# Performance work log

Hardware: AMD Instinct MI355X
Metric: run time of the kernel (lower is better)

The kernel has to match this reference:

```python
import jax, jax.numpy as jnp
import numpy as np

EPS = 1e-8
C_RGLRU = 8.0  # Griffin constant

def rmsnorm(x, w):
    rms = jnp.sqrt(jnp.mean(x * x, axis=-1, keepdims=True) + EPS)
    return w * (x / rms)

def causal_depthwise_conv(x, conv_w, conv_b):
    # x: [B,S,H], conv_w: [K,H] depthwise causal conv, left-padded
    K = conv_w.shape[0]
    S = x.shape[1]
    xp = jnp.pad(x, ((0, 0), (K - 1, 0), (0, 0)))
    y = sum(conv_w[k] * xp[:, k:k + S, :] for k in range(K))
    return y + conv_b

def rg_lru(x, ga_W, ga_b, gx_W, gx_b, a_param):
    # x: [B,S,H]. Griffin RG-LRU: h_t = a_t h_{t-1} + sqrt(1-a_t^2) (i_t * x_t)
    r = jax.nn.sigmoid(x @ ga_W + ga_b)          # recurrence gate
    i = jax.nn.sigmoid(x @ gx_W + gx_b)          # input gate
    log_a = -C_RGLRU * jax.nn.softplus(a_param) * r
    a = jnp.exp(log_a)
    mult = jnp.sqrt(-jnp.expm1(2.0 * log_a))     # sqrt(1 - a^2), stable
    b = mult * (i * x)
    def combine(c1, c2):
        a1, b1 = c1
        a2, b2 = c2
        return a1 * a2, a2 * b1 + b2
    _, h = jax.lax.associative_scan(combine, (a, b), axis=1)
    return h

def setup_inputs() -> dict:
    D, H, F, K, B, S = 2048, 2048, 6144, 4, 2, 2048
    key = jax.random.key(0)
    ks = jax.random.split(key, 16)
    def lin(k, fan_in, shape):
        return jax.random.normal(k, shape, jnp.float32) * (fan_in ** -0.5)
    return {
        "x": jax.random.normal(ks[0], (B, S, D), jnp.float32),
        "norm1_w": jnp.ones((D,), jnp.float32),
        "left_W": lin(ks[1], D, (D, H)), "left_b": jnp.zeros((H,), jnp.float32),
        "right_W": lin(ks[2], D, (D, H)), "right_b": jnp.zeros((H,), jnp.float32),
        "conv_w": lin(ks[3], K, (K, H)), "conv_b": jnp.zeros((H,), jnp.float32),
        "ga_W": lin(ks[4], H, (H, H)), "ga_b": jnp.zeros((H,), jnp.float32),
        "gx_W": lin(ks[5], H, (H, H)), "gx_b": jnp.zeros((H,), jnp.float32),
        "a_param": jax.random.uniform(ks[6], (H,), jnp.float32, 0.5, 3.0),
        "out_W": lin(ks[7], H, (H, D)), "out_b": jnp.zeros((D,), jnp.float32),
        "norm2_w": jnp.ones((D,), jnp.float32),
        "up1_W": lin(ks[8], D, (D, F)), "up1_b": jnp.zeros((F,), jnp.float32),
        "up2_W": lin(ks[9], D, (D, F)), "up2_b": jnp.zeros((F,), jnp.float32),
        "down_W": lin(ks[10], F, (F, D)), "down_b": jnp.zeros((D,), jnp.float32),
    }

def reference(x, norm1_w, left_W, left_b, right_W, right_b, conv_w, conv_b,
              ga_W, ga_b, gx_W, gx_b, a_param, out_W, out_b,
              norm2_w, up1_W, up1_b, up2_W, up2_b, down_W, down_b):
    gelu = lambda t: jax.nn.gelu(t, approximate=False)
    # recurrent sub-block (pre-norm residual)
    xn = rmsnorm(x, norm1_w)
    left = gelu(xn @ left_W + left_b)
    right = rg_lru(causal_depthwise_conv(xn @ right_W + right_b, conv_w, conv_b),
                   ga_W, ga_b, gx_W, gx_b, a_param)
    x1 = (left * right) @ out_W + out_b + x
    # gated MLP sub-block (pre-norm residual)
    x1n = rmsnorm(x1, norm2_w)
    mlp = (gelu(x1n @ up1_W + up1_b) * (x1n @ up2_W + up2_b)) @ down_W + down_b
    return mlp + x1
```

## Files before the change

### kernel.cpp

```cpp
#include <hip/hip_runtime.h>
#include <cstdint>
#include <cstdio>

typedef __bf16 bf16x8 __attribute__((ext_vector_type(8)));
typedef float  f32x4  __attribute__((ext_vector_type(4)));
typedef const __attribute__((address_space(1))) void* gas_ptr;
typedef __attribute__((address_space(3))) void* las_ptr;

__device__ __forceinline__ uint16_t f32_to_bf16_rne(float f){
  uint32_t u = __builtin_bit_cast(uint32_t, f);
  u += 0x7FFFu + ((u >> 16) & 1u);
  return (uint16_t)(u >> 16);
}
__device__ __forceinline__ float bf16_to_f32(uint16_t h){
  uint32_t u = (uint32_t)h << 16;
  return __builtin_bit_cast(float, u);
}
__device__ __forceinline__ float gelu_exact(float x){
  return 0.5f * x * (1.f + erff(x * 0.7071067811865475f));
}

template<int EPI>
__device__ __forceinline__ void epi_store(float v, size_t idx, int row, int col,
    int N, int SPLIT, const float* auxF, const uint16_t* auxB,
    float* Cf, uint16_t* Cb0, uint16_t* Cb1, bool second)
{
  if constexpr (EPI == 1) {
    if (!second) Cb0[(size_t)row * SPLIT + col] = f32_to_bf16_rne(gelu_exact(v));
    else         Cb1[(size_t)row * (N - SPLIT) + (col - SPLIT)] = f32_to_bf16_rne(v);
  }
  if constexpr (EPI == 2) Cb0[idx] = f32_to_bf16_rne(v);
  if constexpr (EPI == 4) Cb0[idx] = f32_to_bf16_rne(v + auxF[idx]);
  if constexpr (EPI == 5) Cf[idx] = v + bf16_to_f32(auxB[idx]);
}

template<int EPI, int BM>
__global__ __launch_bounds__(512)
void gemm8p(const uint16_t* __restrict__ A, const uint16_t* __restrict__ Bt,
            const float* __restrict__ bias0, const float* __restrict__ bias1,
            const float* __restrict__ auxF, const uint16_t* __restrict__ auxB,
            float* __restrict__ Cf, uint16_t* __restrict__ Cb0, uint16_t* __restrict__ Cb1,
            int M, int N, int K, int SPLIT)
{
  constexpr int BN = 256;
  constexpr int M_REP   = BM / 32;
  constexpr int MH      = M_REP / 2;
  constexpr int LOADS_A = BM / 64;
  constexpr int LOADS_B = BN / 64;
  constexpr int LTOT    = LOADS_A + LOADS_B;
  constexpr int ASIZE   = BM * 128;
  constexpr int ABYTES  = 2 * ASIZE;
  constexpr int BSIZE   = BN * 128;
  __shared__ alignas(16) char smem[2 * (BM + BN) * 128];

  const int tid = threadIdx.x, lane = tid & 63, wid = tid >> 6;
  const int wm = wid >> 2, wn = wid & 3;
  const int la = lane & 15, lq = lane >> 4;
  const int n0 = blockIdx.x * BN, m0 = blockIdx.y * BM;

  const int rt = tid >> 3;
  const int gs = (tid & 7) ^ (rt & 7);
  const uint16_t* srcA = A  + (size_t)(m0 + rt) * K + gs * 8;
  const uint16_t* srcB = Bt + (size_t)(n0 + rt) * K + gs * 8;

  const int rowAb = (wm * (BM / 2) + la) * 128;
  const int rowBb = (wn * 64 + la) * 128;
  const int ck0 = ((lq)     ^ (la & 7)) * 16;
  const int ck1 = ((4 + lq) ^ (la & 7)) * 16;

  f32x4 acc[M_REP][4];
  const f32x4 fz = {0.f, 0.f, 0.f, 0.f};
#pragma unroll
  for (int m = 0; m < M_REP; ++m)
#pragma unroll
    for (int n = 0; n < 4; ++n) acc[m][n] = fz;

  bf16x8 aF[MH][2], bF0[2][2], bF1[2][2];
  const int NT = K >> 6;

#define STAGE_A8(KT, BUF) do { _Pragma("unroll")                              \
    for (int l = 0; l < LOADS_A; ++l)                                         \
      __builtin_amdgcn_global_load_lds(                                       \
          (gas_ptr)(srcA + (size_t)(KT) * 64 + (size_t)l * 64 * K),           \
          (las_ptr)(smem + (BUF) * ASIZE + (l * 512 + tid) * 16), 16, 0, 0);  \
  } while (0)
#define STAGE_B8(KT, BUF) do { _Pragma("unroll")                              \
    for (int l = 0; l < LOADS_B; ++l)                                         \
      __builtin_amdgcn_global_load_lds(                                       \
          (gas_ptr)(srcB + (size_t)(KT) * 64 + (size_t)l * 64 * K),           \
          (las_ptr)(smem + ABYTES + (BUF) * BSIZE + (l * 512 + tid) * 16),    \
          16, 0, 0);                                                          \
  } while (0)
#define RD_B8(DST, NH, BUF) do { _Pragma("unroll")                            \
    for (int nq = 0; nq < 2; ++nq) {                                          \
      int ro_ = ABYTES + (BUF) * BSIZE + rowBb + ((NH) * 2 + nq) * 2048;      \
      DST[nq][0] = *(const bf16x8*)(smem + ro_ + ck0);                        \
      DST[nq][1] = *(const bf16x8*)(smem + ro_ + ck1);                        \
    }                                                                         \
  } while (0)
#define RD_A8(MHS, BUF) do { _Pragma("unroll")                                \
    for (int mq = 0; mq < MH; ++mq) {                                         \
      int ro_ = (BUF) * ASIZE + rowAb + ((MHS) * MH + mq) * 2048;             \
      aF[mq][0] = *(const bf16x8*)(smem + ro_ + ck0);                         \
      aF[mq][1] = *(const bf16x8*)(smem + ro_ + ck1);                         \
    }                                                                         \
  } while (0)
#define MM8(MHS, NH, BF) do { _Pragma("unroll")                               \
    for (int mq = 0; mq < MH; ++mq)                                           \
      _Pragma("unroll")                                                       \
      for (int nq = 0; nq < 2; ++nq) {                                        \
        acc[(MHS)*MH+mq][(NH)*2+nq] = __builtin_amdgcn_mfma_f32_16x16x32_bf16(\
            aF[mq][0], BF[nq][0], acc[(MHS)*MH+mq][(NH)*2+nq], 0, 0, 0);      \
        acc[(MHS)*MH+mq][(NH)*2+nq] = __builtin_amdgcn_mfma_f32_16x16x32_bf16(\
            aF[mq][1], BF[nq][1], acc[(MHS)*MH+mq][(NH)*2+nq], 0, 0, 0);      \
      }                                                                       \
  } while (0)
#define BARR() __builtin_amdgcn_s_barrier()

  STAGE_A8(0, 0); STAGE_B8(0, 0);
  STAGE_A8(1, 1); STAGE_B8(1, 1);
  asm volatile("s_waitcnt vmcnt(%0)" :: "i"(LTOT) : "memory");
  BARR();

  for (int t = 0; t < NT; ++t) {
    const int buf = t & 1;
    const bool pf = (t + 2 < NT);
    RD_B8(bF0, 0, buf); RD_A8(0, buf);
    asm volatile("s_waitcnt lgkmcnt(8)" ::: "memory");
    BARR();
    __builtin_amdgcn_s_setprio(1); MM8(0, 0, bF0); __builtin_amdgcn_s_setprio(0);
    BARR();
    RD_B8(bF1, 1, buf);
    BARR();
    __builtin_amdgcn_s_setprio(1); MM8(0, 1, bF1); __builtin_amdgcn_s_setprio(0);
    BARR();
    RD_A8(1, buf);
    if (pf) STAGE_B8(t + 2, buf);
    BARR();
    __builtin_amdgcn_s_setprio(1); MM8(1, 0, bF0); __builtin_amdgcn_s_setprio(0);
    BARR();
    if (pf) STAGE_A8(t + 2, buf);
    BARR();
    __builtin_amdgcn_s_setprio(1); MM8(1, 1, bF1); __builtin_amdgcn_s_setprio(0);
    if (pf) asm volatile("s_waitcnt vmcnt(%0)" :: "i"(LTOT) : "memory");
    else    asm volatile("s_waitcnt vmcnt(0)" ::: "memory");
    BARR();
  }
#undef STAGE_A8
#undef STAGE_B8
#undef RD_B8
#undef RD_A8
#undef MM8
#undef BARR

  if constexpr (EPI == 6) {
    const int GN = N >> 1;
#pragma unroll
    for (int np = 0; np < 2; ++np) {
      int gcol = (n0 >> 1) + wn * 32 + np * 16 + la;
      float b1 = bias0[gcol], b2 = bias1[gcol];
#pragma unroll
      for (int m = 0; m < M_REP; ++m) {
        int rbase = m0 + wm * (BM / 2) + m * 16 + lq * 4;
#pragma unroll
        for (int r = 0; r < 4; ++r) {
          int row = rbase + r;
          float v1 = acc[m][2*np][r] + b1;
          float v2 = acc[m][2*np+1][r] + b2;
          Cb0[(size_t)row * GN + gcol] = f32_to_bf16_rne(gelu_exact(v1) * v2);
        }
      }
    }
  } else {
#pragma unroll
    for (int n = 0; n < 4; ++n) {
      int col = n0 + wn * 64 + n * 16 + la;
      const bool second = (col >= SPLIT);
      float bv = second ? bias1[col - SPLIT] : bias0[col];
#pragma unroll
      for (int m = 0; m < M_REP; ++m) {
        int rbase = m0 + wm * (BM / 2) + m * 16 + lq * 4;
#pragma unroll
        for (int r = 0; r < 4; ++r) {
          int row = rbase + r;
          size_t idx = (size_t)row * N + col;
          epi_store<EPI>(acc[m][n][r] + bv, idx, row, col, N, SPLIT, auxF, auxB, Cf, Cb0, Cb1, second);
        }
      }
    }
  }
}

template<int EPI, int BM>
__global__ __launch_bounds__(512)
void gemm2p(const uint16_t* __restrict__ A, const uint16_t* __restrict__ Bt,
            const float* __restrict__ bias0, const float* __restrict__ bias1,
            const float* __restrict__ auxF, const uint16_t* __restrict__ auxB,
            float* __restrict__ Cf, uint16_t* __restrict__ Cb0, uint16_t* __restrict__ Cb1,
            int M, int N, int K, int SPLIT)
{
  constexpr int BN = 256;
  constexpr int M_REP   = BM / 32;
  constexpr int LOADS_A = BM / 64;
  constexpr int LOADS_B = BN / 64;
  constexpr int ABYTES  = 2 * BM * 128;
  __shared__ alignas(16) char smem[2 * (BM + BN) * 128];

  const int tid  = threadIdx.x;
  const int lane = tid & 63;
  const int wid  = tid >> 6;
  const int wm = wid >> 2, wn = wid & 3;
  const int la = lane & 15, lq = lane >> 4;
  const int n0 = blockIdx.x * BN;
  const int m0 = blockIdx.y * BM;

  const int rt = tid >> 3;
  const int gs = (tid & 7) ^ (rt & 7);
  const uint16_t* srcA = A  + (size_t)(m0 + rt) * K + gs * 8;
  const uint16_t* srcB = Bt + (size_t)(n0 + rt) * K + gs * 8;

  const int rowAb = (wm * (BM / 2) + la) * 128;
  const int rowBb = (wn * 64 + la) * 128;
  const int ck0 = ((lq)     ^ (la & 7)) * 16;
  const int ck1 = ((4 + lq) ^ (la & 7)) * 16;

  f32x4 acc[M_REP][4];
  const f32x4 fz = {0.f, 0.f, 0.f, 0.f};
#pragma unroll
  for (int m = 0; m < M_REP; ++m)
#pragma unroll
    for (int n = 0; n < 4; ++n) acc[m][n] = fz;

  const int NT = K >> 6;

#define STAGE(KT, BUF) do {                                                   \
    const uint16_t* sa_ = srcA + (size_t)(KT) * 64;                           \
    const uint16_t* sb_ = srcB + (size_t)(KT) * 64;                           \
    _Pragma("unroll")                                                         \
    for (int l = 0; l < LOADS_A; ++l)                                         \
      __builtin_amdgcn_global_load_lds((gas_ptr)(sa_ + (size_t)l * 64 * K),   \
          (las_ptr)(smem + (BUF) * BM * 128 + (l * 512 + tid) * 16), 16, 0, 0);\
    _Pragma("unroll")                                                         \
    for (int l = 0; l < LOADS_B; ++l)                                         \
      __builtin_amdgcn_global_load_lds((gas_ptr)(sb_ + (size_t)l * 64 * K),   \
          (las_ptr)(smem + ABYTES + (BUF) * BN * 128 + (l * 512 + tid) * 16), \
          16, 0, 0);                                                          \
  } while (0)

  STAGE(0, 0);
  asm volatile("s_waitcnt vmcnt(0)" ::: "memory");
  __builtin_amdgcn_s_barrier();

  int cur = 0;
  for (int kt = 0; kt < NT; ++kt) {
    const bool pf = (kt + 1 < NT);
    if (pf) STAGE(kt + 1, cur ^ 1);

    const int offA = cur * BM * 128;
    const int offB = ABYTES + cur * BN * 128;

    bf16x8 bF[4][2];
#pragma unroll
    for (int n = 0; n < 4; ++n) {
      int ro = offB + rowBb + n * 2048;
      bF[n][0] = *(const bf16x8*)(smem + ro + ck0);
      bF[n][1] = *(const bf16x8*)(smem + ro + ck1);
    }
    __builtin_amdgcn_s_setprio(1);
#pragma unroll
    for (int m = 0; m < M_REP; ++m) {
      int ro = offA + rowAb + m * 2048;
      bf16x8 a0 = *(const bf16x8*)(smem + ro + ck0);
      bf16x8 a1 = *(const bf16x8*)(smem + ro + ck1);
#pragma unroll
      for (int n = 0; n < 4; ++n) {
        acc[m][n] = __builtin_amdgcn_mfma_f32_16x16x32_bf16(a0, bF[n][0], acc[m][n], 0, 0, 0);
        acc[m][n] = __builtin_amdgcn_mfma_f32_16x16x32_bf16(a1, bF[n][1], acc[m][n], 0, 0, 0);
      }
    }
    __builtin_amdgcn_s_setprio(0);

    if (pf) {
      asm volatile("s_waitcnt vmcnt(0)" ::: "memory");
      __builtin_amdgcn_s_barrier();
      cur ^= 1;
    }
  }
#undef STAGE

#pragma unroll
  for (int n = 0; n < 4; ++n) {
    int col = n0 + wn * 64 + n * 16 + la;
    const bool second = (col >= SPLIT);
    float bv = second ? bias1[col - SPLIT] : bias0[col];
#pragma unroll
    for (int m = 0; m < M_REP; ++m) {
      int rbase = m0 + wm * (BM / 2) + m * 16 + lq * 4;
#pragma unroll
      for (int r = 0; r < 4; ++r) {
        int row = rbase + r;
        size_t idx = (size_t)row * N + col;
        epi_store<EPI>(acc[m][n][r] + bv, idx, row, col, N, SPLIT, auxF, auxB, Cf, Cb0, Cb1, second);
      }
    }
  }
}

__global__ __launch_bounds__(256)
void cvt_transpose(const float* __restrict__ in, uint16_t* __restrict__ out, int R, int C)
{
  __shared__ float tile[64][65];
  const int r0 = blockIdx.y * 64, c0 = blockIdx.x * 64;
  const int t = threadIdx.x;
  const int lc = (t & 15) * 4;
  const int lr0 = t >> 4;
#pragma unroll
  for (int j = 0; j < 4; j++){
    int lr = lr0 + j*16;
    float4 v = *(const float4*)(in + (size_t)(r0 + lr) * C + c0 + lc);
    tile[lr][lc+0] = v.x; tile[lr][lc+1] = v.y; tile[lr][lc+2] = v.z; tile[lr][lc+3] = v.w;
  }
  __syncthreads();
  const int oc = t >> 2;
  const int rseg = (t & 3) * 16;
  alignas(16) uint16_t tmp[16];
#pragma unroll
  for (int j = 0; j < 16; j++) tmp[j] = f32_to_bf16_rne(tile[rseg + j][oc]);
  uint4* dst = (uint4*)(out + (size_t)(c0 + oc) * R + r0 + rseg);
  dst[0] = *(const uint4*)(&tmp[0]);
  dst[1] = *(const uint4*)(&tmp[8]);
}

__global__ __launch_bounds__(256)
void cvt_transpose_ileave(const float* __restrict__ in, uint16_t* __restrict__ out,
                          int R, int C, int half)
{
  __shared__ float tile[64][65];
  const int r0 = blockIdx.y * 64, c0 = blockIdx.x * 64;
  const int t = threadIdx.x;
  const int lc = (t & 15) * 4;
  const int lr0 = t >> 4;
#pragma unroll
  for (int j = 0; j < 4; j++){
    int lr = lr0 + j*16;
    float4 v = *(const float4*)(in + (size_t)(r0 + lr) * C + c0 + lc);
    tile[lr][lc+0] = v.x; tile[lr][lc+1] = v.y; tile[lr][lc+2] = v.z; tile[lr][lc+3] = v.w;
  }
  __syncthreads();
  const int oc = t >> 2;
  const int rseg = (t & 3) * 16;
  const int c = c0 + oc;
  const int wrow = ((c >> 4) << 5) + half * 16 + (c & 15);
  alignas(16) uint16_t tmp[16];
#pragma unroll
  for (int j = 0; j < 16; j++) tmp[j] = f32_to_bf16_rne(tile[rseg + j][oc]);
  uint4* dst = (uint4*)(out + (size_t)wrow * R + r0 + rseg);
  dst[0] = *(const uint4*)(&tmp[0]);
  dst[1] = *(const uint4*)(&tmp[8]);
}

__global__ __launch_bounds__(256)
void rmsnorm_kernel(const float* __restrict__ x, const float* __restrict__ w,
                    uint16_t* __restrict__ out, int D)
{
  const int row = blockIdx.x;
  const float* xr = x + (size_t)row * D;
  const int base = threadIdx.x * 8;
  float4 va = *(const float4*)(xr + base);
  float4 vb = *(const float4*)(xr + base + 4);
  float ss = va.x*va.x + va.y*va.y + va.z*va.z + va.w*va.w
           + vb.x*vb.x + vb.y*vb.y + vb.z*vb.z + vb.w*vb.w;
#pragma unroll
  for (int o = 32; o > 0; o >>= 1) ss += __shfl_xor(ss, o);
  __shared__ float red[4];
  if ((threadIdx.x & 63) == 0) red[threadIdx.x >> 6] = ss;
  __syncthreads();
  float tot = red[0] + red[1] + red[2] + red[3];
  float inv = rsqrtf(tot / (float)D + 1e-8f);
  float4 wa = *(const float4*)(w + base);
  float4 wb = *(const float4*)(w + base + 4);
  alignas(16) uint16_t tmp[8];
  tmp[0] = f32_to_bf16_rne(va.x * wa.x * inv);
  tmp[1] = f32_to_bf16_rne(va.y * wa.y * inv);
  tmp[2] = f32_to_bf16_rne(va.z * wa.z * inv);
  tmp[3] = f32_to_bf16_rne(va.w * wa.w * inv);
  tmp[4] = f32_to_bf16_rne(vb.x * wb.x * inv);
  tmp[5] = f32_to_bf16_rne(vb.y * wb.y * inv);
  tmp[6] = f32_to_bf16_rne(vb.z * wb.z * inv);
  tmp[7] = f32_to_bf16_rne(vb.w * wb.w * inv);
  *(uint4*)(out + (size_t)row * D + base) = *(const uint4*)tmp;
}

__global__ __launch_bounds__(256)
void rmsnorm_bf16_kernel(const uint16_t* __restrict__ x, const float* __restrict__ w,
                         uint16_t* __restrict__ out, int D)
{
  const int row = blockIdx.x;
  const uint16_t* xr = x + (size_t)row * D;
  const int base = threadIdx.x * 8;
  uint4 v = *(const uint4*)(xr + base);
  const uint16_t* vp = (const uint16_t*)&v;
  float xs[8];
  float ss = 0.f;
#pragma unroll
  for (int j = 0; j < 8; ++j){ xs[j] = bf16_to_f32(vp[j]); ss += xs[j]*xs[j]; }
#pragma unroll
  for (int o = 32; o > 0; o >>= 1) ss += __shfl_xor(ss, o);
  __shared__ float red[4];
  if ((threadIdx.x & 63) == 0) red[threadIdx.x >> 6] = ss;
  __syncthreads();
  float tot = red[0] + red[1] + red[2] + red[3];
  float inv = rsqrtf(tot / (float)D + 1e-8f);
  float4 wa = *(const float4*)(w + base);
  float4 wb = *(const float4*)(w + base + 4);
  float wv[8] = {wa.x, wa.y, wa.z, wa.w, wb.x, wb.y, wb.z, wb.w};
  alignas(16) uint16_t tmp[8];
#pragma unroll
  for (int j = 0; j < 8; ++j) tmp[j] = f32_to_bf16_rne(xs[j] * wv[j] * inv);
  *(uint4*)(out + (size_t)row * D + base) = *(const uint4*)tmp;
}

__global__ __launch_bounds__(256)
void conv_kernel(const uint16_t* __restrict__ xin, const float* __restrict__ cw,
                 const float* __restrict__ cb, uint16_t* __restrict__ yout,
                 int S, int H)
{
  const int h = blockIdx.x * 256 + threadIdx.x;
  const int b = blockIdx.z;
  const int t0 = blockIdx.y * 128;
  const float w0 = cw[h], w1 = cw[H + h], w2 = cw[2*H + h], w3 = cw[3*H + h];
  const float bias = cb[h];
  const size_t colbase = (size_t)b * S * H + h;
  float xm3 = (t0 >= 3) ? bf16_to_f32(xin[colbase + (size_t)(t0-3)*H]) : 0.f;
  float xm2 = (t0 >= 2) ? bf16_to_f32(xin[colbase + (size_t)(t0-2)*H]) : 0.f;
  float xm1 = (t0 >= 1) ? bf16_to_f32(xin[colbase + (size_t)(t0-1)*H]) : 0.f;
  for (int t = t0; t < t0 + 128; ++t){
    size_t idx = colbase + (size_t)t * H;
    float xt = bf16_to_f32(xin[idx]);
    float y = w0*xm3 + w1*xm2 + w2*xm1 + w3*xt + bias;
    yout[idx] = f32_to_bf16_rne(y);
    xm3 = xm2; xm2 = xm1; xm1 = xt;
  }
}

__device__ __forceinline__ void rglru_ab(float rp, float ip, float xc, float coef,
                                         float& a, float& bb)
{
  float r  = 1.f / (1.f + expf(-rp));
  float la = coef * r;
  a = expf(la);
  float mult = sqrtf(-expm1f(2.f * la));
  float ig = 1.f / (1.f + expf(-ip));
  bb = mult * ig * xc;
}

__global__ __launch_bounds__(256)
void scan_phase1(const uint16_t* __restrict__ gpre, const uint16_t* __restrict__ convb,
                 const float* __restrict__ ap,
                 float* __restrict__ SA, float* __restrict__ SB,
                 int S, int H, int T0, int NC)
{
  const int h = blockIdx.x * 256 + threadIdx.x;
  const int j = blockIdx.y, b = blockIdx.z;
  const float coef = -8.f * log1pf(expf(ap[h]));
  size_t rowb = (size_t)b * S + (size_t)j * T0;
  float A = 1.f, Bc = 0.f;
  for (int t = 0; t < T0; ++t){
    size_t row = rowb + t;
    float rp = bf16_to_f32(gpre[row * 2 * H + h]);
    float ip = bf16_to_f32(gpre[row * 2 * H + H + h]);
    float xc = bf16_to_f32(convb[row * H + h]);
    float a, bb; rglru_ab(rp, ip, xc, coef, a, bb);
    A *= a; Bc = a * Bc + bb;
  }
  size_t o = ((size_t)b * NC + j) * H + h;
  SA[o] = A; SB[o] = Bc;
}

__global__ __launch_bounds__(256)
void scan_phase2(const float* __restrict__ SA, const float* __restrict__ SB,
                 float* __restrict__ SH, int H, int NC)
{
  const int h = blockIdx.x * 256 + threadIdx.x;
  const int b = blockIdx.y;
  float hh = 0.f;
  for (int j = 0; j < NC; ++j){
    size_t o = ((size_t)b * NC + j) * H + h;
    SH[o] = hh;
    hh = SA[o] * hh + SB[o];
  }
}

__global__ __launch_bounds__(256)
void scan_phase3(const uint16_t* __restrict__ gpre, const uint16_t* __restrict__ convb,
                 const float* __restrict__ ap, const float* __restrict__ SH,
                 const uint16_t* __restrict__ left, uint16_t* __restrict__ lr,
                 int S, int H, int T0, int NC)
{
  const int h = blockIdx.x * 256 + threadIdx.x;
  const int j = blockIdx.y, b = blockIdx.z;
  const float coef = -8.f * log1pf(expf(ap[h]));
  float hh = SH[((size_t)b * NC + j) * H + h];
  size_t rowb = (size_t)b * S + (size_t)j * T0;
  for (int t = 0; t < T0; ++t){
    size_t row = rowb + t;
    float rp = bf16_to_f32(gpre[row * 2 * H + h]);
    float ip = bf16_to_f32(gpre[row * 2 * H + H + h]);
    float xc = bf16_to_f32(convb[row * H + h]);
    float a, bb; rglru_ab(rp, ip, xc, coef, a, bb);
    hh = a * hh + bb;
    lr[row * H + h] = f32_to_bf16_rne(bf16_to_f32(left[row * H + h]) * hh);
  }
}

extern "C" void kernel_launch(void* const* d_in, const int* in_sizes, int n_in,
                              void* d_out, int out_size, void* d_ws, size_t ws_size,
                              hipStream_t stream)
{
  const int B = 2, S = 2048, D = 2048, H = 2048, F = 6144;
  const int M = B * S;
  const int NC = 32, T0 = S / NC;

  const float* x       = (const float*)d_in[0];
  const float* norm1_w = (const float*)d_in[1];
  const float* left_W  = (const float*)d_in[2];
  const float* left_b  = (const float*)d_in[3];
  const float* right_W = (const float*)d_in[4];
  const float* right_b = (const float*)d_in[5];
  const float* conv_w  = (const float*)d_in[6];
  const float* conv_b  = (const float*)d_in[7];
  const float* ga_W    = (const float*)d_in[8];
  const float* ga_b    = (const float*)d_in[9];
  const float* gx_W    = (const float*)d_in[10];
  const float* gx_b    = (const float*)d_in[11];
  const float* a_param = (const float*)d_in[12];
  const float* out_W   = (const float*)d_in[13];
  const float* out_b   = (const float*)d_in[14];
  const float* norm2_w = (const float*)d_in[15];
  const float* up1_W   = (const float*)d_in[16];
  const float* up1_b   = (const float*)d_in[17];
  const float* up2_W   = (const float*)d_in[18];
  const float* up2_b   = (const float*)d_in[19];
  const float* down_W  = (const float*)d_in[20];
  const float* down_b  = (const float*)d_in[21];

  char* ws = (char*)d_ws;
  size_t off = 0;
  auto alloc = [&](size_t bytes) -> char* {
    char* p = ws + off; off += (bytes + 255) & ~(size_t)255; return p;
  };
  uint16_t* WT    = (uint16_t*)alloc((size_t)2 * F * D * 2);
  uint16_t* XN    = (uint16_t*)alloc((size_t)M * D * 2);
  uint16_t* LEFT  = (uint16_t*)alloc((size_t)M * H * 2);
  uint16_t* RPRE  = (uint16_t*)alloc((size_t)M * H * 2);
  uint16_t* CONVB = (uint16_t*)alloc((size_t)M * H * 2);
  uint16_t* GPRE  = (uint16_t*)alloc((size_t)M * 2 * H * 2);
  uint16_t* LR    = (uint16_t*)alloc((size_t)M * H * 2);
  uint16_t* X1B   = (uint16_t*)alloc((size_t)M * D * 2);
  uint16_t* X1N   = (uint16_t*)alloc((size_t)M * D * 2);
  float*    SA    = (float*)   alloc((size_t)B * NC * H * 4);
  float*    SB    = (float*)   alloc((size_t)B * NC * H * 4);
  float*    SHB   = (float*)   alloc((size_t)B * NC * H * 4);
  uint16_t* G     = XN;

  if (off > ws_size) {
    fprintf(stderr, "kernel_launch: ws too small, need %zu have %zu\n", off, ws_size);
    return;
  }

  float* OUT = (float*)d_out;
  dim3 blk(256);
  dim3 gblk(512);

  rmsnorm_kernel<<<M, blk, 0, stream>>>(x, norm1_w, XN, D);

  cvt_transpose<<<dim3(H/64, D/64), blk, 0, stream>>>(left_W, WT, D, H);
  cvt_transpose<<<dim3(H/64, D/64), blk, 0, stream>>>(right_W, WT + (size_t)H * D, D, H);
  gemm8p<1, 256><<<dim3((2*H)/256, M/256), gblk, 0, stream>>>(
      XN, WT, left_b, right_b, nullptr, nullptr, nullptr, LEFT, RPRE, M, 2*H, D, H);

  conv_kernel<<<dim3(H/256, S/128, B), blk, 0, stream>>>(RPRE, conv_w, conv_b, CONVB, S, H);

  cvt_transpose<<<dim3(H/64, H/64), blk, 0, stream>>>(ga_W, WT, H, H);
  cvt_transpose<<<dim3(H/64, H/64), blk, 0, stream>>>(gx_W, WT + (size_t)H * H, H, H);
  gemm8p<2, 256><<<dim3((2*H)/256, M/256), gblk, 0, stream>>>(
      CONVB, WT, ga_b, gx_b, nullptr, nullptr, nullptr, GPRE, nullptr, M, 2*H, H, H);

  scan_phase1<<<dim3(H/256, NC, B), blk, 0, stream>>>(GPRE, CONVB, a_param, SA, SB, S, H, T0, NC);
  scan_phase2<<<dim3(H/256, B), blk, 0, stream>>>(SA, SB, SHB, H, NC);
  scan_phase3<<<dim3(H/256, NC, B), blk, 0, stream>>>(GPRE, CONVB, a_param, SHB, LEFT, LR, S, H, T0, NC);

  cvt_transpose<<<dim3(D/64, H/64), blk, 0, stream>>>(out_W, WT, H, D);
  gemm2p<4, 128><<<dim3(D/256, M/128), gblk, 0, stream>>>(
      LR, WT, out_b, out_b, x, nullptr, nullptr, X1B, nullptr, M, D, H, D);

  rmsnorm_bf16_kernel<<<M, blk, 0, stream>>>(X1B, norm2_w, X1N, D);

  cvt_transpose_ileave<<<dim3(F/64, D/64), blk, 0, stream>>>(up1_W, WT, D, F, 0);
  cvt_transpose_ileave<<<dim3(F/64, D/64), blk, 0, stream>>>(up2_W, WT, D, F, 1);
  gemm8p<6, 256><<<dim3((2*F)/256, M/256), gblk, 0, stream>>>(
      X1N, WT, up1_b, up2_b, nullptr, nullptr, nullptr, G, nullptr, M, 2*F, D, 2*F);

  cvt_transpose<<<dim3(D/64, F/64), blk, 0, stream>>>(down_W, WT, F, D);
  gemm2p<5, 128><<<dim3(D/256, M/128), gblk, 0, stream>>>(
      G, WT, down_b, down_b, nullptr, X1B, OUT, nullptr, nullptr, M, D, F, D);
}
```

Measured before the change: 736.5 us.

## Split-K down projection on 8-wave GEMM with separate reduce kernel

Replaces the BM=128 down-projection GEMM with the larger BM=256 gemm8p variant. It splits K=6144 in two halves across blockIdx.z, keeping the block count at 256. Each half writes fp32 partials into reused workspace (CONVB/GPRE/LR region), and a new vectorized reduce kernel sums them and adds the bias and bf16 residual. This aims for better tile reuse and pipelining in the heaviest GEMM, at the cost of roughly 128MB of extra fp32 partial traffic and one more launch.

After: 745.2 us (median of 2 runs). No clear change (+1.2%).

```diff
diff --git a/kernel.cpp b/kernel.cpp
--- a/kernel.cpp
+++ b/kernel.cpp
@@ -32,6 +32,7 @@
   if constexpr (EPI == 2) Cb0[idx] = f32_to_bf16_rne(v);
   if constexpr (EPI == 4) Cb0[idx] = f32_to_bf16_rne(v + auxF[idx]);
   if constexpr (EPI == 5) Cf[idx] = v + bf16_to_f32(auxB[idx]);
+  if constexpr (EPI == 7) Cf[idx] = v;
 }
 
 template<int EPI, int BM>
@@ -58,10 +59,13 @@
   const int la = lane & 15, lq = lane >> 4;
   const int n0 = blockIdx.x * BN, m0 = blockIdx.y * BM;
 
+  const int kst = (EPI == 7) ? SPLIT : K;
+  const size_t kbase = (EPI == 7) ? (size_t)blockIdx.z * K : 0;
+
   const int rt = tid >> 3;
   const int gs = (tid & 7) ^ (rt & 7);
-  const uint16_t* srcA = A  + (size_t)(m0 + rt) * K + gs * 8;
-  const uint16_t* srcB = Bt + (size_t)(n0 + rt) * K + gs * 8;
+  const uint16_t* srcA = A  + (size_t)(m0 + rt) * kst + kbase + gs * 8;
+  const uint16_t* srcB = Bt + (size_t)(n0 + rt) * kst + kbase + gs * 8;
 
   const int rowAb = (wm * (BM / 2) + la) * 128;
   const int rowBb = (wn * 64 + la) * 128;
@@ -81,13 +85,13 @@
 #define STAGE_A8(KT, BUF) do { _Pragma("unroll")                              \
     for (int l = 0; l < LOADS_A; ++l)                                         \
       __builtin_amdgcn_global_load_lds(                                       \
-          (gas_ptr)(srcA + (size_t)(KT) * 64 + (size_t)l * 64 * K),           \
+          (gas_ptr)(srcA + (size_t)(KT) * 64 + (size_t)l * 64 * kst),         \
           (las_ptr)(smem + (BUF) * ASIZE + (l * 512 + tid) * 16), 16, 0, 0);  \
   } while (0)
 #define STAGE_B8(KT, BUF) do { _Pragma("unroll")                              \
     for (int l = 0; l < LOADS_B; ++l)                                         \
       __builtin_amdgcn_global_load_lds(                                       \
-          (gas_ptr)(srcB + (size_t)(KT) * 64 + (size_t)l * 64 * K),           \
+          (gas_ptr)(srcB + (size_t)(KT) * 64 + (size_t)l * 64 * kst),         \
           (las_ptr)(smem + ABYTES + (BUF) * BSIZE + (l * 512 + tid) * 16),    \
           16, 0, 0);                                                          \
   } while (0)
@@ -172,18 +176,21 @@
       }
     }
   } else {
+    const size_t zoff = (EPI == 7) ? (size_t)blockIdx.z * M * N : 0;
 #pragma unroll
     for (int n = 0; n < 4; ++n) {
       int col = n0 + wn * 64 + n * 16 + la;
-      const bool second = (col >= SPLIT);
-      float bv = second ? bias1[col - SPLIT] : bias0[col];
+      const bool second = (col >= SPLIT) && (EPI != 7);
+      float bv;
+      if constexpr (EPI == 7) bv = 0.f;
+      else bv = second ? bias1[col - SPLIT] : bias0[col];
 #pragma unroll
       for (int m = 0; m < M_REP; ++m) {
         int rbase = m0 + wm * (BM / 2) + m * 16 + lq * 4;
 #pragma unroll
         for (int r = 0; r < 4; ++r) {
           int row = rbase + r;
-          size_t idx = (size_t)row * N + col;
+          size_t idx = zoff + (size_t)row * N + col;
           epi_store<EPI>(acc[m][n][r] + bv, idx, row, col, N, SPLIT, auxF, auxB, Cf, Cb0, Cb1, second);
         }
       }
@@ -304,6 +311,32 @@
       }
     }
   }
+}
+
+__global__ __launch_bounds__(256)
+void reduce_splitk(const float* __restrict__ P, const float* __restrict__ bias,
+                   const uint16_t* __restrict__ x1, float* __restrict__ out,
+                   int N, size_t total)
+{
+  size_t i = ((size_t)blockIdx.x * 256 + threadIdx.x) * 8;
+  int col = (int)(i % (size_t)N);
+  float4 a0 = *(const float4*)(P + i);
+  float4 a1 = *(const float4*)(P + i + 4);
+  float4 b0 = *(const float4*)(P + total + i);
+  float4 b1 = *(const float4*)(P + total + i + 4);
+  float4 w0 = *(const float4*)(bias + col);
+  float4 w1 = *(const float4*)(bias + col + 4);
+  uint4 xv = *(const uint4*)(x1 + i);
+  const uint16_t* xp = (const uint16_t*)&xv;
+  float o[8];
+  o[0] = a0.x + b0.x + w0.x; o[1] = a0.y + b0.y + w0.y;
+  o[2] = a0.z + b0.z + w0.z; o[3] = a0.w + b0.w + w0.w;
+  o[4] = a1.x + b1.x + w1.x; o[5] = a1.y + b1.y + w1.y;
+  o[6] = a1.z + b1.z + w1.z; o[7] = a1.w + b1.w + w1.w;
+#pragma unroll
+  for (int j = 0; j < 8; ++j) o[j] += bf16_to_f32(xp[j]);
+  *(float4*)(out + i)     = *(const float4*)(&o[0]);
+  *(float4*)(out + i + 4) = *(const float4*)(&o[4]);
 }
 
 __global__ __launch_bounds__(256)
@@ -562,6 +595,7 @@
   float*    SB    = (float*)   alloc((size_t)B * NC * H * 4);
   float*    SHB   = (float*)   alloc((size_t)B * NC * H * 4);
   uint16_t* G     = XN;
+  float*    PART  = (float*)CONVB;
 
   if (off > ws_size) {
     fprintf(stderr, "kernel_launch: ws too small, need %zu have %zu\n", off, ws_size);
@@ -602,6 +636,8 @@
       X1N, WT, up1_b, up2_b, nullptr, nullptr, nullptr, G, nullptr, M, 2*F, D, 2*F);
 
   cvt_transpose<<<dim3(D/64, F/64), blk, 0, stream>>>(down_W, WT, F, D);
-  gemm2p<5, 128><<<dim3(D/256, M/128), gblk, 0, stream>>>(
-      G, WT, down_b, down_b, nullptr, X1B, OUT, nullptr, nullptr, M, D, F, D);
-}
+  gemm8p<7, 256><<<dim3(D/256, M/256, 2), gblk, 0, stream>>>(
+      G, WT, down_b, down_b, nullptr, nullptr, PART, nullptr, nullptr, M, D, F/2, F);
+  reduce_splitk<<<dim3((unsigned)((size_t)M * D / 8 / 256)), blk, 0, stream>>>(
+      PART, down_b, X1B, OUT, D, (size_t)M * D);
+}
```
